# Kernel tuning notes

Measured on AMD Instinct MI355X. Metric: run time of the kernel, lower is better.

## Reference

```python
import jax, jax.numpy as jnp
import numpy as np

N_NODES = 100000
N_EDGES = 3200000
F_IN = 512
F_HID = 32
N_CLASSES = 16


def gcn_conv(x, edge_index, W, b):
    """PyG GCNConv: symmetric-normalized aggregation with self-loops.
    out_i = sum_{j->i} (d_j d_i)^{-1/2} (x_j W) + d_i^{-1} (x_i W) + b
    where d_i = in-degree(i) + 1 (self-loop included)."""
    n = x.shape[0]
    h = x @ W  # [N, F_out]
    src, dst = edge_index[0], edge_index[1]
    deg = jax.ops.segment_sum(jnp.ones_like(src, dtype=h.dtype), dst,
                              num_segments=n) + 1.0  # self-loop
    dinv = jax.lax.rsqrt(deg)  # [N]
    norm = dinv[src] * dinv[dst]  # [E]
    msg = h[src] * norm[:, None]  # [E, F_out]
    agg = jax.ops.segment_sum(msg, dst, num_segments=n)
    # self-loop contribution: norm_ii = dinv_i^2
    agg = agg + h * (dinv * dinv)[:, None]
    return agg + b


def setup_inputs() -> dict:
    key = jax.random.key(0)
    k1, k2, k3, k4 = jax.random.split(key, 4)
    x = jax.random.normal(k1, (N_NODES, F_IN), dtype=jnp.float32)
    edge_index = jax.random.randint(k2, (2, N_EDGES), 0, N_NODES, dtype=jnp.int64)
    W1 = jax.random.normal(k3, (F_IN, F_HID), dtype=jnp.float32) / np.sqrt(F_IN)
    b1 = jnp.zeros((F_HID,), dtype=jnp.float32)
    W2 = jax.random.normal(k4, (F_HID, N_CLASSES), dtype=jnp.float32) / np.sqrt(F_HID)
    b2 = jnp.zeros((N_CLASSES,), dtype=jnp.float32)
    return {"x": x, "edge_index": edge_index, "W1": W1, "b1": b1, "W2": W2, "b2": b2}


def reference(x, edge_index, W1, b1, W2, b2):
    h = jax.nn.relu(gcn_conv(x, edge_index, W1, b1))
    # F.dropout(training=self.training) is identity in eval mode
    h = gcn_conv(h, edge_index, W2, b2)
    return jax.nn.log_softmax(h, axis=1)
```

## Files before the change

### kernel.cpp

```cpp
#include <hip/hip_runtime.h>
#include <cstdint>
#include <cstddef>

#define F_IN 512
#define F_HID 32
#define N_CLS 16
#define BSH 9
#define BNODES (1 << BSH)
#define CAP 20480

typedef __attribute__((ext_vector_type(4))) float f32x4;
typedef __attribute__((ext_vector_type(8))) __bf16 bf16x8;

__device__ __forceinline__ float4 shfl_xor_f4(float4 v, int mask) {
    v.x = __shfl_xor(v.x, mask, 64);
    v.y = __shfl_xor(v.y, mask, 64);
    v.z = __shfl_xor(v.z, mask, 64);
    v.w = __shfl_xor(v.w, mask, 64);
    return v;
}

__device__ __forceinline__ short bf16s(float f) {
    unsigned u = __float_as_uint(f);
    return (short)((u + 0x7FFFu + ((u >> 16) & 1u)) >> 16);
}

__global__ __launch_bounds__(256) void k_detect(const int* e, int* flag, int* bcur,
                                                int nbuk) {
    __shared__ int zc;
    int t = threadIdx.x;
    if (t == 0) zc = 0;
    __syncthreads();
    int z = 0;
#pragma unroll
    for (int j = 0; j < 4; ++j)
        if (e[2 * (t * 4 + j) + 1] == 0) z++;
    if (z) atomicAdd(&zc, z);
    for (int i = t; i < nbuk; i += 256) bcur[i] = i * CAP;
    __syncthreads();
    if (t == 0) *flag = (zc >= 1016) ? 1 : 0;
}

__global__ __launch_bounds__(256) void k_wcvt(const float* __restrict__ W,
                                              uint4* __restrict__ Wfrag) {
    int i = blockIdx.x * 256 + threadIdx.x;
    int s = i >> 7, rem = i & 127, h = rem >> 6, l = rem & 63;
    int g = l >> 4, c = 16 * h + (l & 15);
    unsigned p[4];
#pragma unroll
    for (int q = 0; q < 4; ++q) {
        int k0 = 32 * s + 8 * g + 2 * q;
        unsigned lo = (unsigned short)bf16s(W[(size_t)k0 * F_HID + c]);
        unsigned hi = (unsigned short)bf16s(W[(size_t)(k0 + 1) * F_HID + c]);
        p[q] = lo | (hi << 16);
    }
    Wfrag[i] = make_uint4(p[0], p[1], p[2], p[3]);
}

__device__ __forceinline__ int edge_get(const void* e, int is64, long long idx) {
    return is64 ? (int)((const long long*)e)[idx] : ((const int*)e)[idx];
}

#define SK 16
__global__ __launch_bounds__(256) void k_bscatter(const void* edges, const int* flag,
                                                  int* bcur, int* __restrict__ bucket,
                                                  int E, int nbuk) {
    __shared__ int h[256], sbase[256];
    int t = threadIdx.x;
    if (t < nbuk) h[t] = 0;
    __syncthreads();
    int is64 = *flag;
    long long base = (long long)blockIdx.x * 256 * SK;
    int ss[SK], dd[SK], rk[SK];
#pragma unroll
    for (int j = 0; j < SK; ++j) {
        long long i = base + j * 256 + t;
        if (i < E) {
            dd[j] = edge_get(edges, is64, (long long)E + i);
            ss[j] = edge_get(edges, is64, i);
            rk[j] = atomicAdd(&h[dd[j] >> BSH], 1);
        } else dd[j] = -1;
    }
    __syncthreads();
    if (t < nbuk && h[t]) sbase[t] = atomicAdd(&bcur[t], h[t]);
    __syncthreads();
#pragma unroll
    for (int j = 0; j < SK; ++j) {
        if (dd[j] >= 0) {
            int b = dd[j] >> BSH;
            int pos = sbase[b] + rk[j];
            if (pos < (b + 1) * CAP)
                bucket[pos] = ((dd[j] & (BNODES - 1)) << 17) | ss[j];
        }
    }
}

__global__ __launch_bounds__(512) void k_build(const int* __restrict__ bucket,
                                               const int* __restrict__ bcur,
                                               int* __restrict__ rbeg,
                                               int* __restrict__ rend,
                                               float* __restrict__ dinv,
                                               int* __restrict__ csr, int N) {
    __shared__ int cnt[512];
    __shared__ int wsum[8];
    int b = blockIdx.x;
    int t = threadIdx.x;
    int nb0 = b << BSH;
    int beg = b * CAP, end = bcur[b];
    cnt[t] = 0;
    __syncthreads();
    for (int e = beg + t; e < end; e += 512)
        atomicAdd(&cnt[bucket[e] >> 17], 1);
    __syncthreads();
    int v = cnt[t];
    int lane = t & 63, w = t >> 6;
    int inc = v;
#pragma unroll
    for (int off = 1; off < 64; off <<= 1) {
        int u = __shfl_up(inc, off, 64);
        if (lane >= off) inc += u;
    }
    if (lane == 63) wsum[w] = inc;
    __syncthreads();
    int wo = 0;
#pragma unroll
    for (int k = 0; k < 8; ++k)
        if (k < w) wo += wsum[k];
    int excl = inc - v + wo;
    int node = nb0 + t;
    if (node < N) {
        rbeg[node] = beg + excl;
        rend[node] = beg + excl + v;
        dinv[node] = rsqrtf((float)v + 1.0f);
    }
    __syncthreads();
    cnt[t] = beg + excl;
    __syncthreads();
    for (int e = beg + t; e < end; e += 512) {
        int p = bucket[e];
        int pos = atomicAdd(&cnt[p >> 17], 1);
        csr[pos] = p & 0x1FFFF;
    }
}

__global__ __launch_bounds__(256) void k_gemm1(const float* __restrict__ x,
                                               const uint4* __restrict__ Wfrag,
                                               const float* __restrict__ dinv,
                                               float* __restrict__ hs1, int N) {
    __shared__ uint4 wf[2048];
    int t = threadIdx.x;
#pragma unroll
    for (int j = 0; j < 8; ++j) wf[t + j * 256] = Wfrag[t + j * 256];
    __syncthreads();

    int w = t >> 6, l = t & 63;
    int c = l & 15, g = l >> 4;
    int wrow = blockIdx.x * 64 + w * 16;
    int row = wrow + c;
    if (row >= N) row = N - 1;
    const float4* xp = (const float4*)(x + (size_t)row * F_IN + 8 * g);

    f32x4 acc0 = {0.f, 0.f, 0.f, 0.f};
    f32x4 acc1 = {0.f, 0.f, 0.f, 0.f};

    float4 A[4], B[4];
#pragma unroll
    for (int j = 0; j < 4; ++j) { A[j] = xp[8 * j]; B[j] = xp[8 * j + 1]; }

#pragma unroll
    for (int s = 0; s < 16; ++s) {
        const int j = s & 3;
        float4 a0 = A[j], a1 = B[j];
        if (s < 12) { A[j] = xp[8 * (s + 4)]; B[j] = xp[8 * (s + 4) + 1]; }
        bf16x8 av;
        av[0] = (__bf16)a0.x; av[1] = (__bf16)a0.y;
        av[2] = (__bf16)a0.z; av[3] = (__bf16)a0.w;
        av[4] = (__bf16)a1.x; av[5] = (__bf16)a1.y;
        av[6] = (__bf16)a1.z; av[7] = (__bf16)a1.w;
        bf16x8 b0 = __builtin_bit_cast(bf16x8, wf[s * 128 + l]);
        bf16x8 b1 = __builtin_bit_cast(bf16x8, wf[s * 128 + 64 + l]);
        acc0 = __builtin_amdgcn_mfma_f32_16x16x32_bf16(av, b0, acc0, 0, 0, 0);
        acc1 = __builtin_amdgcn_mfma_f32_16x16x32_bf16(av, b1, acc1, 0, 0, 0);
    }

#pragma unroll
    for (int r = 0; r < 4; ++r) {
        int ro = wrow + g * 4 + r;
        if (ro < N) {
            float di = dinv[ro];
            hs1[(size_t)ro * F_HID + c]      = acc0[r] * di;
            hs1[(size_t)ro * F_HID + 16 + c] = acc1[r] * di;
        }
    }
}

__global__ __launch_bounds__(256) void k_gather1(const float* __restrict__ hs1,
                                                 const int* __restrict__ csr,
                                                 const int* __restrict__ rbeg,
                                                 const int* __restrict__ rend,
                                                 const float* __restrict__ dinv,
                                                 const float* __restrict__ b1,
                                                 const float* __restrict__ W2,
                                                 float* __restrict__ hs2, int N) {
    __shared__ float w2s[32][17];
    int t = threadIdx.x;
    for (int i = t; i < 512; i += 256) w2s[i >> 4][i & 15] = W2[i];
    __syncthreads();
    int node = blockIdx.x * 4 + (t >> 6);
    if (node >= N) return;
    int lane = t & 63;
    int g = lane >> 3, l = lane & 7;
    const float4* h4 = (const float4*)hs1;
    int beg = rbeg[node], end = rend[node];
    float4 a = make_float4(0.f, 0.f, 0.f, 0.f);
    for (int e = beg + g; e < end; e += 8) {
        int src = csr[e];
        float4 v = h4[(size_t)src * 8 + l];
        a.x += v.x; a.y += v.y; a.z += v.z; a.w += v.w;
    }
    float4 u;
    u = shfl_xor_f4(a, 8);  a.x += u.x; a.y += u.y; a.z += u.z; a.w += u.w;
    u = shfl_xor_f4(a, 16); a.x += u.x; a.y += u.y; a.z += u.z; a.w += u.w;
    u = shfl_xor_f4(a, 32); a.x += u.x; a.y += u.y; a.z += u.z; a.w += u.w;
    float4 self = h4[(size_t)node * 8 + l];
    float di = dinv[node];
    float4 bb = ((const float4*)b1)[l];
    float4 r;
    r.x = fmaxf(di * (a.x + self.x) + bb.x, 0.f);
    r.y = fmaxf(di * (a.y + self.y) + bb.y, 0.f);
    r.z = fmaxf(di * (a.z + self.z) + bb.z, 0.f);
    r.w = fmaxf(di * (a.w + self.w) + bb.w, 0.f);
    int k0 = 4 * l, c0 = 2 * g;
    float p0 = r.x * w2s[k0][c0]     + r.y * w2s[k0 + 1][c0]
             + r.z * w2s[k0 + 2][c0] + r.w * w2s[k0 + 3][c0];
    float p1 = r.x * w2s[k0][c0 + 1]     + r.y * w2s[k0 + 1][c0 + 1]
             + r.z * w2s[k0 + 2][c0 + 1] + r.w * w2s[k0 + 3][c0 + 1];
    p0 += __shfl_xor(p0, 1, 64); p1 += __shfl_xor(p1, 1, 64);
    p0 += __shfl_xor(p0, 2, 64); p1 += __shfl_xor(p1, 2, 64);
    p0 += __shfl_xor(p0, 4, 64); p1 += __shfl_xor(p1, 4, 64);
    if (l == 0)
        *(float2*)(hs2 + (size_t)node * N_CLS + c0) = make_float2(p0 * di, p1 * di);
}

__global__ __launch_bounds__(256) void k_gather2(const float* __restrict__ hs2,
                                                 const int* __restrict__ csr,
                                                 const int* __restrict__ rbeg,
                                                 const int* __restrict__ rend,
                                                 const float* __restrict__ dinv,
                                                 const float* __restrict__ b2,
                                                 float* __restrict__ out, int N) {
    int node = blockIdx.x * 4 + (threadIdx.x >> 6);
    if (node >= N) return;
    int lane = threadIdx.x & 63;
    int g = lane >> 2, l = lane & 3;
    const float4* h4 = (const float4*)hs2;
    int beg = rbeg[node], end = rend[node];
    float4 a = make_float4(0.f, 0.f, 0.f, 0.f);
    for (int e = beg + g; e < end; e += 16) {
        int src = csr[e];
        float4 v = h4[(size_t)src * 4 + l];
        a.x += v.x; a.y += v.y; a.z += v.z; a.w += v.w;
    }
    float4 u;
    u = shfl_xor_f4(a, 4);  a.x += u.x; a.y += u.y; a.z += u.z; a.w += u.w;
    u = shfl_xor_f4(a, 8);  a.x += u.x; a.y += u.y; a.z += u.z; a.w += u.w;
    u = shfl_xor_f4(a, 16); a.x += u.x; a.y += u.y; a.z += u.z; a.w += u.w;
    u = shfl_xor_f4(a, 32); a.x += u.x; a.y += u.y; a.z += u.z; a.w += u.w;
    if (g == 0) {
        float4 self = h4[(size_t)node * 4 + l];
        float di = dinv[node];
        float4 bb = ((const float4*)b2)[l];
        float4 v;
        v.x = di * (a.x + self.x) + bb.x;
        v.y = di * (a.y + self.y) + bb.y;
        v.z = di * (a.z + self.z) + bb.z;
        v.w = di * (a.w + self.w) + bb.w;
        float m = fmaxf(fmaxf(v.x, v.y), fmaxf(v.z, v.w));
        m = fmaxf(m, __shfl_xor(m, 1, 64));
        m = fmaxf(m, __shfl_xor(m, 2, 64));
        float s = __expf(v.x - m) + __expf(v.y - m) + __expf(v.z - m) + __expf(v.w - m);
        s += __shfl_xor(s, 1, 64);
        s += __shfl_xor(s, 2, 64);
        float ls = m + __logf(s);
        float4 r = make_float4(v.x - ls, v.y - ls, v.z - ls, v.w - ls);
        ((float4*)out)[(size_t)node * 4 + l] = r;
    }
}

extern "C" void kernel_launch(void* const* d_in, const int* in_sizes, int n_in,
                              void* d_out, int out_size, void* d_ws, size_t ws_size,
                              hipStream_t stream) {
    const float* x  = (const float*)d_in[0];
    const void* edges = d_in[1];
    const float* W1 = (const float*)d_in[2];
    const float* b1 = (const float*)d_in[3];
    const float* W2 = (const float*)d_in[4];
    const float* b2 = (const float*)d_in[5];
    float* out = (float*)d_out;

    const int N = in_sizes[0] / F_IN;
    const int E = in_sizes[1] / 2;
    const int NBUK = (N + BNODES - 1) >> BSH;

    char* w = (char*)d_ws;
    size_t off = 0;
    auto take = [&](size_t bytes) {
        size_t o = off;
        off += (bytes + 15) & ~(size_t)15;
        return o;
    };
    float* hs1    = (float*)(w + take((size_t)N * F_HID * 4));
    float* hs2    = (float*)(w + take((size_t)N * N_CLS * 4));
    float* dinv   = (float*)(w + take((size_t)N * 4));
    int* rbeg     = (int*)(w + take((size_t)N * 4));
    int* rend     = (int*)(w + take((size_t)N * 4));
    int* bucket   = (int*)(w + take((size_t)NBUK * CAP * 4));
    int* csr      = (int*)(w + take((size_t)NBUK * CAP * 4));
    uint4* Wfrag  = (uint4*)(w + take(2048 * 16));
    int* bcur     = (int*)(w + take(1024));
    int* flag     = (int*)(w + take(16));

    hipLaunchKernelGGL(k_detect, dim3(1), dim3(256), 0, stream, (const int*)edges, flag, bcur, NBUK);
    hipLaunchKernelGGL(k_wcvt, dim3(8), dim3(256), 0, stream, W1, Wfrag);
    const int SB = (E + 256 * SK - 1) / (256 * SK);
    hipLaunchKernelGGL(k_bscatter, dim3(SB), dim3(256), 0, stream, edges, flag, bcur, bucket, E, NBUK);
    hipLaunchKernelGGL(k_build, dim3(NBUK), dim3(512), 0, stream, bucket, bcur, rbeg, rend, dinv, csr, N);
    hipLaunchKernelGGL(k_gemm1, dim3((N + 63) / 64), dim3(256), 0, stream, x, Wfrag, dinv, hs1, N);
    hipLaunchKernelGGL(k_gather1, dim3((N + 3) / 4), dim3(256), 0, stream, hs1, csr, rbeg, rend, dinv, b1, W2, hs2, N);
    hipLaunchKernelGGL(k_gather2, dim3((N + 3) / 4), dim3(256), 0, stream, hs2, csr, rbeg, rend, dinv, b2, out, N);
}
```

Baseline: 228.9 us.

## Fuse edge bucketing with first GEMM and move dinv scaling into CSR build

New measurement: 205.4 us. 10.3% less time.

```diff
diff --git a/kernel.cpp b/kernel.cpp
--- a/kernel.cpp
+++ b/kernel.cpp
@@ -8,6 +8,7 @@
 #define BSH 9
 #define BNODES (1 << BSH)
 #define CAP 20480
+#define SK 16
 
 typedef __attribute__((ext_vector_type(4))) float f32x4;
 typedef __attribute__((ext_vector_type(8))) __bf16 bf16x8;
@@ -61,36 +62,86 @@
     return is64 ? (int)((const long long*)e)[idx] : ((const int*)e)[idx];
 }
 
-#define SK 16
-__global__ __launch_bounds__(256) void k_bscatter(const void* edges, const int* flag,
-                                                  int* bcur, int* __restrict__ bucket,
-                                                  int E, int nbuk) {
-    __shared__ int h[256], sbase[256];
+__global__ __launch_bounds__(256) void k_fused(const float* __restrict__ x,
+                                               const uint4* __restrict__ Wfrag,
+                                               float* __restrict__ hs1, int N,
+                                               const void* edges, const int* flag,
+                                               int* bcur, int* __restrict__ bucket,
+                                               int E, int nbuk, int SB) {
+    __shared__ uint4 wf[2048];
     int t = threadIdx.x;
-    if (t < nbuk) h[t] = 0;
-    __syncthreads();
-    int is64 = *flag;
-    long long base = (long long)blockIdx.x * 256 * SK;
-    int ss[SK], dd[SK], rk[SK];
-#pragma unroll
-    for (int j = 0; j < SK; ++j) {
-        long long i = base + j * 256 + t;
-        if (i < E) {
-            dd[j] = edge_get(edges, is64, (long long)E + i);
-            ss[j] = edge_get(edges, is64, i);
-            rk[j] = atomicAdd(&h[dd[j] >> BSH], 1);
-        } else dd[j] = -1;
-    }
-    __syncthreads();
-    if (t < nbuk && h[t]) sbase[t] = atomicAdd(&bcur[t], h[t]);
-    __syncthreads();
-#pragma unroll
-    for (int j = 0; j < SK; ++j) {
-        if (dd[j] >= 0) {
-            int b = dd[j] >> BSH;
-            int pos = sbase[b] + rk[j];
-            if (pos < (b + 1) * CAP)
-                bucket[pos] = ((dd[j] & (BNODES - 1)) << 17) | ss[j];
+
+    if ((int)blockIdx.x < SB) {
+        int* h = (int*)wf;
+        int* sbase = h + 256;
+        if (t < nbuk) h[t] = 0;
+        __syncthreads();
+        int is64 = *flag;
+        long long base = (long long)blockIdx.x * 256 * SK;
+        int ss[SK], dd[SK], rk[SK];
+#pragma unroll
+        for (int j = 0; j < SK; ++j) {
+            long long i = base + j * 256 + t;
+            if (i < E) {
+                dd[j] = edge_get(edges, is64, (long long)E + i);
+                ss[j] = edge_get(edges, is64, i);
+                rk[j] = atomicAdd(&h[dd[j] >> BSH], 1);
+            } else dd[j] = -1;
+        }
+        __syncthreads();
+        if (t < nbuk && h[t]) sbase[t] = atomicAdd(&bcur[t], h[t]);
+        __syncthreads();
+#pragma unroll
+        for (int j = 0; j < SK; ++j) {
+            if (dd[j] >= 0) {
+                int b = dd[j] >> BSH;
+                int pos = sbase[b] + rk[j];
+                if (pos < (b + 1) * CAP)
+                    bucket[pos] = ((dd[j] & (BNODES - 1)) << 17) | ss[j];
+            }
+        }
+    } else {
+#pragma unroll
+        for (int j = 0; j < 8; ++j) wf[t + j * 256] = Wfrag[t + j * 256];
+        __syncthreads();
+        int tile = blockIdx.x - SB;
+        int w = t >> 6, l = t & 63;
+        int c = l & 15, g = l >> 4;
+        int wrow = tile * 64 + w * 16;
+        int row = wrow + c;
+        if (row >= N) row = N - 1;
+        const float4* xp = (const float4*)(x + (size_t)row * F_IN + 8 * g);
+
+        f32x4 acc0 = {0.f, 0.f, 0.f, 0.f};
+        f32x4 acc1 = {0.f, 0.f, 0.f, 0.f};
+
+        float4 A[4], B[4];
+#pragma unroll
+        for (int j = 0; j < 4; ++j) { A[j] = xp[8 * j]; B[j] = xp[8 * j + 1]; }
+
+#pragma unroll
+        for (int s = 0; s < 16; ++s) {
+            const int j = s & 3;
+            float4 a0 = A[j], a1 = B[j];
+            if (s < 12) { A[j] = xp[8 * (s + 4)]; B[j] = xp[8 * (s + 4) + 1]; }
+            bf16x8 av;
+            av[0] = (__bf16)a0.x; av[1] = (__bf16)a0.y;
+            av[2] = (__bf16)a0.z; av[3] = (__bf16)a0.w;
+            av[4] = (__bf16)a1.x; av[5] = (__bf16)a1.y;
+            av[6] = (__bf16)a1.z; av[7] = (__bf16)a1.w;
+            bf16x8 b0 = __builtin_bit_cast(bf16x8, wf[s * 128 + l]);
+            bf16x8 b1 = __builtin_bit_cast(bf16x8, wf[s * 128 + 64 + l]);
+            acc0 = __builtin_amdgcn_mfma_f32_16x16x32_bf16(av, b0, acc0, 0, 0, 0);
+            acc1 = __builtin_amdgcn_mfma_f32_16x16x32_bf16(av, b1, acc1, 0, 0, 0);
+        }
+
+#pragma unroll
+        for (int r = 0; r < 4; ++r) {
+            int ro = wrow + g * 4 + r;
+            if (ro < N) {
+                hs1[(size_t)ro * F_HID + c]      = acc0[r];
+                hs1[(size_t)ro * F_HID + 16 + c] = acc1[r];
+            }
         }
     }
 }
@@ -100,9 +151,11 @@
                                                int* __restrict__ rbeg,
                                                int* __restrict__ rend,
                                                float* __restrict__ dinv,
-                                               int* __restrict__ csr, int N) {
+                                               int* __restrict__ csr,
+                                               float* __restrict__ hs1, int N) {
     __shared__ int cnt[512];
     __shared__ int wsum[8];
+    __shared__ float sdinv[512];
     int b = blockIdx.x;
     int t = threadIdx.x;
     int nb0 = b << BSH;
@@ -128,10 +181,12 @@
         if (k < w) wo += wsum[k];
     int excl = inc - v + wo;
     int node = nb0 + t;
+    float d = rsqrtf((float)v + 1.0f);
+    sdinv[t] = d;
     if (node < N) {
         rbeg[node] = beg + excl;
         rend[node] = beg + excl + v;
-        dinv[node] = rsqrtf((float)v + 1.0f);
+        dinv[node] = d;
     }
     __syncthreads();
     cnt[t] = beg + excl;
@@ -141,55 +196,14 @@
         int pos = atomicAdd(&cnt[p >> 17], 1);
         csr[pos] = p & 0x1FFFF;
     }
-}
-
-__global__ __launch_bounds__(256) void k_gemm1(const float* __restrict__ x,
-                                               const uint4* __restrict__ Wfrag,
-                                               const float* __restrict__ dinv,
-                                               float* __restrict__ hs1, int N) {
-    __shared__ uint4 wf[2048];
-    int t = threadIdx.x;
-#pragma unroll
-    for (int j = 0; j < 8; ++j) wf[t + j * 256] = Wfrag[t + j * 256];
-    __syncthreads();
-
-    int w = t >> 6, l = t & 63;
-    int c = l & 15, g = l >> 4;
-    int wrow = blockIdx.x * 64 + w * 16;
-    int row = wrow + c;
-    if (row >= N) row = N - 1;
-    const float4* xp = (const float4*)(x + (size_t)row * F_IN + 8 * g);
-
-    f32x4 acc0 = {0.f, 0.f, 0.f, 0.f};
-    f32x4 acc1 = {0.f, 0.f, 0.f, 0.f};
-
-    float4 A[4], B[4];
-#pragma unroll
-    for (int j = 0; j < 4; ++j) { A[j] = xp[8 * j]; B[j] = xp[8 * j + 1]; }
-
-#pragma unroll
-    for (int s = 0; s < 16; ++s) {
-        const int j = s & 3;
-        float4 a0 = A[j], a1 = B[j];
-        if (s < 12) { A[j] = xp[8 * (s + 4)]; B[j] = xp[8 * (s + 4) + 1]; }
-        bf16x8 av;
-        av[0] = (__bf16)a0.x; av[1] = (__bf16)a0.y;
-        av[2] = (__bf16)a0.z; av[3] = (__bf16)a0.w;
-        av[4] = (__bf16)a1.x; av[5] = (__bf16)a1.y;
-        av[6] = (__bf16)a1.z; av[7] = (__bf16)a1.w;
-        bf16x8 b0 = __builtin_bit_cast(bf16x8, wf[s * 128 + l]);
-        bf16x8 b1 = __builtin_bit_cast(bf16x8, wf[s * 128 + 64 + l]);
-        acc0 = __builtin_amdgcn_mfma_f32_16x16x32_bf16(av, b0, acc0, 0, 0, 0);
-        acc1 = __builtin_amdgcn_mfma_f32_16x16x32_bf16(av, b1, acc1, 0, 0, 0);
-    }
-
-#pragma unroll
-    for (int r = 0; r < 4; ++r) {
-        int ro = wrow + g * 4 + r;
-        if (ro < N) {
-            float di = dinv[ro];
-            hs1[(size_t)ro * F_HID + c]      = acc0[r] * di;
-            hs1[(size_t)ro * F_HID + 16 + c] = acc1[r] * di;
+    float4* h1 = (float4*)hs1 + (size_t)nb0 * 8;
+    for (int j = t; j < 4096; j += 512) {
+        int n2 = nb0 + (j >> 3);
+        if (n2 < N) {
+            float dv = sdinv[j >> 3];
+            float4 vv = h1[j];
+            vv.x *= dv; vv.y *= dv; vv.z *= dv; vv.w *= dv;
+            h1[j] = vv;
         }
     }
 }
@@ -213,8 +227,11 @@
     const float4* h4 = (const float4*)hs1;
     int beg = rbeg[node], end = rend[node];
     float4 a = make_float4(0.f, 0.f, 0.f, 0.f);
-    for (int e = beg + g; e < end; e += 8) {
-        int src = csr[e];
+    int e = beg + g;
+    int nsrc = (e < end) ? csr[e] : 0;
+    for (; e < end; e += 8) {
+        int src = nsrc;
+        if (e + 8 < end) nsrc = csr[e + 8];
         float4 v = h4[(size_t)src * 8 + l];
         a.x += v.x; a.y += v.y; a.z += v.z; a.w += v.w;
     }
@@ -256,8 +273,11 @@
     const float4* h4 = (const float4*)hs2;
     int beg = rbeg[node], end = rend[node];
     float4 a = make_float4(0.f, 0.f, 0.f, 0.f);
-    for (int e = beg + g; e < end; e += 16) {
-        int src = csr[e];
+    int e = beg + g;
+    int nsrc = (e < end) ? csr[e] : 0;
+    for (; e < end; e += 16) {
+        int src = nsrc;
+        if (e + 16 < end) nsrc = csr[e + 16];
         float4 v = h4[(size_t)src * 4 + l];
         a.x += v.x; a.y += v.y; a.z += v.z; a.w += v.w;
     }
@@ -323,9 +343,10 @@
     hipLaunchKernelGGL(k_detect, dim3(1), dim3(256), 0, stream, (const int*)edges, flag, bcur, NBUK);
     hipLaunchKernelGGL(k_wcvt, dim3(8), dim3(256), 0, stream, W1, Wfrag);
     const int SB = (E + 256 * SK - 1) / (256 * SK);
-    hipLaunchKernelGGL(k_bscatter, dim3(SB), dim3(256), 0, stream, edges, flag, bcur, bucket, E, NBUK);
-    hipLaunchKernelGGL(k_build, dim3(NBUK), dim3(512), 0, stream, bucket, bcur, rbeg, rend, dinv, csr, N);
-    hipLaunchKernelGGL(k_gemm1, dim3((N + 63) / 64), dim3(256), 0, stream, x, Wfrag, dinv, hs1, N);
+    const int NT = (N + 63) / 64;
+    hipLaunchKernelGGL(k_fused, dim3(SB + NT), dim3(256), 0, stream,
+                       x, Wfrag, hs1, N, edges, flag, bcur, bucket, E, NBUK, SB);
+    hipLaunchKernelGGL(k_build, dim3(NBUK), dim3(512), 0, stream, bucket, bcur, rbeg, rend, dinv, csr, hs1, N);
     hipLaunchKernelGGL(k_gather1, dim3((N + 3) / 4), dim3(256), 0, stream, hs1, csr, rbeg, rend, dinv, b1, W2, hs2, N);
     hipLaunchKernelGGL(k_gather2, dim3((N + 3) / 4), dim3(256), 0, stream, hs2, csr, rbeg, rend, dinv, b2, out, N);
 }
```
